# Performance work log

Hardware: AMD Instinct MI355X
Metric: run time of the kernel (lower is better)

## Reference

```python
import jax, jax.numpy as jnp
import numpy as np

EMBEDDING_BOUND = 1e4  # uniform init bound for box centers (repo constant)


def setup_inputs() -> dict:
    key = jax.random.key(0)
    k1, k2, k3 = jax.random.split(key, 3)
    num_classes, dim = 100000, 50
    d = dim // 2
    # init per MultiBoxEL.init_embeddings: centers ~ U(-B, B), offsets ~ N(1, 0.333)
    centers = jax.random.uniform(k1, (num_classes, d), dtype=jnp.float32,
                                 minval=-EMBEDDING_BOUND, maxval=EMBEDDING_BOUND)
    offsets = 1.0 + 0.333 * jax.random.normal(k2, (num_classes, d), dtype=jnp.float32)
    class_embeds = jnp.concatenate([centers, offsets], axis=1)  # [C, dim]
    nf1_data = jax.random.randint(k3, (2_000_000, 2), 0, num_classes)  # [N, 2] class ids
    return {"class_embeds": class_embeds, "nf1_data": nf1_data}


def _to_box(emb):
    # get_multiboxes: first half = center, second half = |offsets|
    d = emb.shape[-1] // 2
    return emb[:, :d], jnp.abs(emb[:, d:])


def reference(class_embeds, nf1_data):
    """nf1_loss (C subsumed-by D): batched inclusion loss 1 - Area(C ^ D)/Area(C),
    then L2 norm of relu(losses) over the batch (a scalar), exactly as inclusion_loss."""
    c_emb = class_embeds[nf1_data[:, 0]]  # [N, dim] gather (memory-bound)
    d_emb = class_embeds[nf1_data[:, 1]]
    cc, co = _to_box(c_emb)
    dc, do = _to_box(d_emb)
    # box intersection: [max(lowers), min(uppers)]; empty -> side length clipped to 0
    lo = jnp.maximum(cc - co, dc - do)
    hi = jnp.minimum(cc + co, dc + do)
    inter_area = jnp.prod(jax.nn.relu(hi - lo), axis=-1)  # [N]
    c_area = jnp.prod(2.0 * co, axis=-1)                  # [N] box volume = prod(2*offset)
    loss = jnp.where(c_area == 0, 0.0,
           jnp.where(jnp.isinf(c_area), 1.0 - inter_area / (2.0 * EMBEDDING_BOUND),
                     1.0 - inter_area / c_area))
    return jnp.linalg.norm(jax.nn.relu(loss))
```

## Files before the change

kernel.cpp:

```cpp
#include <hip/hip_runtime.h>
#include <hip/hip_cooperative_groups.h>
#include <math.h>

namespace cg = cooperative_groups;


#define DIMS 25
#define EMB_BOUND 10000.0f
#define FBLK 1024

__global__ void init_ws_kernel(float* ws) {
    if (threadIdx.x == 0 && blockIdx.x == 0) ws[0] = 0.0f;
}

__global__ __launch_bounds__(256, 8) void nf1_fallback_kernel(
    const float* __restrict__ emb, const int2* __restrict__ pairs,
    int n_pairs, float* __restrict__ ws)
{
    const int gl  = threadIdx.x & 31;
    const int gid = blockIdx.x * (blockDim.x >> 5) + (threadIdx.x >> 5);
    const int ngrp = gridDim.x * (blockDim.x >> 5);
    float acc = 0.0f;
    for (int p = gid; p < n_pairs; p += ngrp) {
        int2 pr = pairs[p];
        const float* rc = emb + (size_t)pr.x * (2 * DIMS);
        const float* rd = emb + (size_t)pr.y * (2 * DIMS);
        float t = 1.0f, a = 1.0f;
        if (gl < DIMS) {
            float cc = rc[gl], co = fabsf(rc[DIMS + gl]);
            float dc = rd[gl], dd = fabsf(rd[DIMS + gl]);
            float lo = fmaxf(cc - co, dc - dd);
            float hi = fminf(cc + co, dc + dd);
            t = fmaxf(hi - lo, 0.0f);
            a = 2.0f * co;
        }
        #pragma unroll
        for (int m = 16; m >= 1; m >>= 1) { t *= __shfl_xor(t, m, 32); a *= __shfl_xor(a, m, 32); }
        float loss;
        if (a == 0.0f)     loss = 0.0f;
        else if (isinf(a)) loss = 1.0f - t / (2.0f * EMB_BOUND);
        else               loss = 1.0f - t / a;
        loss = fmaxf(loss, 0.0f);
        if (gl == 0) acc += loss * loss;
    }
    #pragma unroll
    for (int m = 32; m >= 1; m >>= 1) acc += __shfl_xor(acc, m, 64);
    __shared__ float wsum[4];
    if ((threadIdx.x & 63) == 0) wsum[threadIdx.x >> 6] = acc;
    __syncthreads();
    if (threadIdx.x == 0) atomicAdd(ws, wsum[0] + wsum[1] + wsum[2] + wsum[3]);
}

__global__ void fallback_finalize_kernel(const float* __restrict__ ws, float* __restrict__ out) {
    if (threadIdx.x == 0 && blockIdx.x == 0) out[0] = sqrtf(fmaxf(ws[0], 0.0f));
}

__device__ __forceinline__ float slow_pair(const float* __restrict__ emb, int2 pr) {
    const float* ra = emb + (size_t)pr.x * (2 * DIMS);
    const float* rb = emb + (size_t)pr.y * (2 * DIMS);
    float inter = 1.0f, carea = 1.0f;
    for (int j = 0; j < DIMS; j++) {
        float cc = ra[j], co = fabsf(ra[DIMS + j]);
        float dc = rb[j], dd = fabsf(rb[DIMS + j]);
        float lo = fmaxf(cc - co, dc - dd);
        float hi = fminf(cc + co, dc + dd);
        inter *= fmaxf(hi - lo, 0.0f);
        carea *= 2.0f * co;
    }
    float loss;
    if (carea == 0.0f)     loss = 0.0f;
    else if (isinf(carea)) loss = 1.0f - inter / (2.0f * EMB_BOUND);
    else                   loss = 1.0f - inter / carea;
    loss = fmaxf(loss, 0.0f);
    return loss * loss;
}

__device__ __forceinline__ float key_pair(const float2* __restrict__ keys,
                                          const float* __restrict__ emb, int2 pr) {
    float2 ka = keys[pr.x];
    float2 kb = keys[pr.y];
    float t0 = fminf(ka.y, kb.y) - fmaxf(ka.x, kb.x);
    if (t0 > 0.0f) return slow_pair(emb, pr);
    return 1.0f;
}

template <int K>
__device__ __forceinline__ int ring_bucket(float lo, float hi) {
    float w = hi - lo;
    if (w <= 16.0f && fabsf(lo) <= 1.0e6f) {
        int i = (int)floorf(lo * 0.0625f);
        int b = i % K; if (b < 0) b += K;
        return b;
    }
    return K;
}

__device__ __forceinline__ bool ring_pass(unsigned a, unsigned b, unsigned K) {
    unsigned dd = (a >= b) ? (a - b) : (b - a);
    return (a == K) | (b == K) | (dd <= 1u) | (dd == K - 1u);
}

__device__ __forceinline__ float screen_pairs(
    const unsigned char* __restrict__ sbuck, const float2* __restrict__ keys,
    const float* __restrict__ emb, const int2* __restrict__ pairs,
    int n_pairs, int t, int nthreads)
{
    float sum = 0.0f;
    const int noct = n_pairs >> 3;
    const int4* p4 = (const int4*)pairs;
    for (int q = t; q < noct; q += nthreads) {
        int4 qa = p4[4 * q + 0], qb = p4[4 * q + 1];
        int4 qc = p4[4 * q + 2], qd = p4[4 * q + 3];
        int2 pr[8] = { make_int2(qa.x, qa.y), make_int2(qa.z, qa.w),
                       make_int2(qb.x, qb.y), make_int2(qb.z, qb.w),
                       make_int2(qc.x, qc.y), make_int2(qc.z, qc.w),
                       make_int2(qd.x, qd.y), make_int2(qd.z, qd.w) };
        unsigned ba[8], bb[8];
        #pragma unroll
        for (int i = 0; i < 8; i++) { ba[i] = sbuck[pr[i].x]; bb[i] = sbuck[pr[i].y]; }
        #pragma unroll
        for (int i = 0; i < 8; i++) {
            if (ring_pass(ba[i], bb[i], 255u)) sum += key_pair(keys, emb, pr[i]);
            else                               sum += 1.0f;
        }
    }
    for (int p = (noct << 3) + t; p < n_pairs; p += nthreads) {
        int2 pr = pairs[p];
        unsigned a = sbuck[pr.x], b = sbuck[pr.y];
        if (ring_pass(a, b, 255u)) sum += key_pair(keys, emb, pr);
        else                       sum += 1.0f;
    }
    return sum;
}

__global__ __launch_bounds__(FBLK, 1) void fused2_kernel(
    const float* __restrict__ emb, float2* __restrict__ keys,
    unsigned char* __restrict__ gbuck, const int2* __restrict__ pairs,
    int n_pairs, int n_rows, float* __restrict__ acc,
    unsigned* __restrict__ ticket, float* __restrict__ out)
{
    extern __shared__ unsigned char sbuck[];
    __shared__ float wsum[FBLK / 64];
    const int nthreads = gridDim.x * blockDim.x;
    const int t = blockIdx.x * blockDim.x + threadIdx.x;
    if (t == 0) { acc[0] = 0.0f; ticket[0] = 0u; }

    for (int r = t; r < n_rows; r += nthreads) {
        float c = emb[(size_t)r * (2 * DIMS)];
        float o = fabsf(emb[(size_t)r * (2 * DIMS) + DIMS]);
        float lo = c - o, hi = c + o;
        keys[r] = make_float2(lo, hi);
        gbuck[r] = (unsigned char)ring_bucket<255>(lo, hi);
    }

    cg::this_grid().sync();

    {
        const int nb16 = (n_rows + 15) >> 4;
        const uint4* g4 = (const uint4*)gbuck;
        uint4* s4 = (uint4*)sbuck;
        for (int i = threadIdx.x; i < nb16; i += blockDim.x) s4[i] = g4[i];
    }
    __syncthreads();

    float sum = screen_pairs(sbuck, keys, emb, pairs, n_pairs, t, nthreads);

    #pragma unroll
    for (int m = 32; m >= 1; m >>= 1) sum += __shfl_xor(sum, m, 64);
    if ((threadIdx.x & 63) == 0) wsum[threadIdx.x >> 6] = sum;
    __syncthreads();
    if (threadIdx.x == 0) {
        float s = 0.0f;
        #pragma unroll
        for (int w = 0; w < FBLK / 64; w++) s += wsum[w];
        atomicAdd(acc, s);
        __threadfence();
        unsigned tk = atomicAdd(ticket, 1u);
        if (tk == gridDim.x - 1)
            out[0] = sqrtf(fmaxf(atomicAdd(acc, 0.0f), 0.0f));
    }
}

__global__ __launch_bounds__(256) void repack_kb_kernel(
    const float* __restrict__ emb, float2* __restrict__ keys,
    unsigned char* __restrict__ gbuck, int n_rows,
    float* __restrict__ acc, unsigned* __restrict__ ticket)
{
    if (blockIdx.x == 0 && threadIdx.x == 0) { acc[0] = 0.0f; ticket[0] = 0u; }
    const int r = blockIdx.x * blockDim.x + threadIdx.x;
    if (r < n_rows) {
        float c = emb[(size_t)r * (2 * DIMS)];
        float o = fabsf(emb[(size_t)r * (2 * DIMS) + DIMS]);
        float lo = c - o, hi = c + o;
        keys[r] = make_float2(lo, hi);
        gbuck[r] = (unsigned char)ring_bucket<255>(lo, hi);
    }
}

__global__ __launch_bounds__(FBLK, 1) void screen_byte2_kernel(
    const float2* __restrict__ keys, const unsigned char* __restrict__ gbuck,
    const float* __restrict__ emb, const int2* __restrict__ pairs,
    int n_pairs, int n_rows, float* __restrict__ acc,
    unsigned* __restrict__ ticket, float* __restrict__ out)
{
    extern __shared__ unsigned char sbuck[];
    __shared__ float wsum[FBLK / 64];
    const int nthreads = gridDim.x * blockDim.x;
    const int t = blockIdx.x * blockDim.x + threadIdx.x;
    {
        const int nb16 = (n_rows + 15) >> 4;
        const uint4* g4 = (const uint4*)gbuck;
        uint4* s4 = (uint4*)sbuck;
        for (int i = threadIdx.x; i < nb16; i += blockDim.x) s4[i] = g4[i];
    }
    __syncthreads();

    float sum = screen_pairs(sbuck, keys, emb, pairs, n_pairs, t, nthreads);

    #pragma unroll
    for (int m = 32; m >= 1; m >>= 1) sum += __shfl_xor(sum, m, 64);
    if ((threadIdx.x & 63) == 0) wsum[threadIdx.x >> 6] = sum;
    __syncthreads();
    if (threadIdx.x == 0) {
        float s = 0.0f;
        #pragma unroll
        for (int w = 0; w < FBLK / 64; w++) s += wsum[w];
        atomicAdd(acc, s);
        __threadfence();
        unsigned tk = atomicAdd(ticket, 1u);
        if (tk == gridDim.x - 1)
            out[0] = sqrtf(fmaxf(atomicAdd(acc, 0.0f), 0.0f));
    }
}

extern "C" void kernel_launch(void* const* d_in, const int* in_sizes, int n_in,
                              void* d_out, int out_size, void* d_ws, size_t ws_size,
                              hipStream_t stream) {
    const float* emb  = (const float*)d_in[0];
    const int2*  prs  = (const int2*)d_in[1];
    int n_pairs = in_sizes[1] / 2;
    int n_rows  = in_sizes[0] / (2 * DIMS);

    float*    ws     = (float*)d_ws;
    unsigned* ticket = (unsigned*)(ws + 1);
    float*    out    = (float*)d_out;
    float2*   keys   = (float2*)((char*)d_ws + 256);
    unsigned char* gbuck = (unsigned char*)(keys + n_rows);

    int dev = 0;  hipGetDevice(&dev);
    int maxShared = 0, coop = 0, numCU = 0;
    hipDeviceGetAttribute(&maxShared, hipDeviceAttributeMaxSharedMemoryPerBlock, dev);
    hipDeviceGetAttribute(&coop, hipDeviceAttributeCooperativeLaunch, dev);
    hipDeviceGetAttribute(&numCU, hipDeviceAttributeMultiprocessorCount, dev);

    const size_t tabBytes = (size_t)((n_rows + 15) & ~15);
    const bool ws_ok = (ws_size >= 256 + (size_t)n_rows * 8 + tabBytes + 64) &&
                       ((n_rows & 1) == 0);
    const bool byte_ok = ((size_t)maxShared >= tabBytes + 512) && ws_ok;

    bool launched = false;
    if (byte_ok && coop && numCU > 0) {
        int blocksPerCU = 0;
        hipError_t oe = hipOccupancyMaxActiveBlocksPerMultiprocessor(
            &blocksPerCU, (const void*)fused2_kernel, FBLK, tabBytes);
        if (oe == hipSuccess && blocksPerCU >= 1) {
            int grid = blocksPerCU * numCU;
            void* args[] = { (void*)&emb, (void*)&keys, (void*)&gbuck,
                             (void*)&prs, (void*)&n_pairs, (void*)&n_rows,
                             (void*)&ws, (void*)&ticket, (void*)&out };
            hipError_t le = hipLaunchCooperativeKernel(
                (const void*)fused2_kernel, dim3(grid), dim3(FBLK),
                args, (unsigned int)tabBytes, stream);
            if (le == hipSuccess) launched = true;
        }
    }

    if (!launched && byte_ok) {
        const int rblocks = (n_rows + 255) / 256;
        hipLaunchKernelGGL(repack_kb_kernel, dim3(rblocks), dim3(256), 0, stream,
                           emb, keys, gbuck, n_rows, ws, ticket);
        const int grid = (numCU > 0) ? numCU : 256;
        hipLaunchKernelGGL(screen_byte2_kernel, dim3(grid), dim3(FBLK),
                           tabBytes, stream,
                           keys, gbuck, emb, prs, n_pairs, n_rows, ws, ticket, out);
        launched = true;
    }

    if (!launched) {
        hipLaunchKernelGGL(init_ws_kernel, dim3(1), dim3(64), 0, stream, ws);
        hipLaunchKernelGGL(nf1_fallback_kernel, dim3(4096), dim3(256), 0, stream,
                           emb, prs, n_pairs, ws);
        hipLaunchKernelGGL(fallback_finalize_kernel, dim3(1), dim3(64), 0, stream, ws, out);
    }
}
```

Baseline: 87.29 us.

## Replace cooperative fused kernel with tiled repack and prefetching screen kernel

Drops the cooperative single-kernel path with a grid-wide sync and goes back to two ordinary launches. The repack kernel now stages 128-row tiles of embeddings in shared memory with coalesced float4 loads, instead of each thread making strided single-float reads. The screen kernel issues its first batch of pair-index loads before filling the shared bucket table, so that load latency overlaps the table copy. The cost is an extra kernel launch boundary in place of the grid sync, plus a fixed grid of 256 blocks.

```diff
diff --git a/kernel.cpp b/kernel.cpp
--- a/kernel.cpp
+++ b/kernel.cpp
@@ -1,13 +1,12 @@
 #include <hip/hip_runtime.h>
-#include <hip/hip_cooperative_groups.h>
 #include <math.h>
-
-namespace cg = cooperative_groups;
 
 
 #define DIMS 25
 #define EMB_BOUND 10000.0f
 #define FBLK 1024
+#define TROWS 128
+#define TFLOATS (TROWS * 2 * DIMS)
 
 __global__ void init_ws_kernel(float* ws) {
     if (threadIdx.x == 0 && blockIdx.x == 0) ws[0] = 0.0f;
@@ -100,104 +99,39 @@
     return (a == K) | (b == K) | (dd <= 1u) | (dd == K - 1u);
 }
 
-__device__ __forceinline__ float screen_pairs(
-    const unsigned char* __restrict__ sbuck, const float2* __restrict__ keys,
-    const float* __restrict__ emb, const int2* __restrict__ pairs,
-    int n_pairs, int t, int nthreads)
-{
-    float sum = 0.0f;
-    const int noct = n_pairs >> 3;
-    const int4* p4 = (const int4*)pairs;
-    for (int q = t; q < noct; q += nthreads) {
-        int4 qa = p4[4 * q + 0], qb = p4[4 * q + 1];
-        int4 qc = p4[4 * q + 2], qd = p4[4 * q + 3];
-        int2 pr[8] = { make_int2(qa.x, qa.y), make_int2(qa.z, qa.w),
-                       make_int2(qb.x, qb.y), make_int2(qb.z, qb.w),
-                       make_int2(qc.x, qc.y), make_int2(qc.z, qc.w),
-                       make_int2(qd.x, qd.y), make_int2(qd.z, qd.w) };
-        unsigned ba[8], bb[8];
-        #pragma unroll
-        for (int i = 0; i < 8; i++) { ba[i] = sbuck[pr[i].x]; bb[i] = sbuck[pr[i].y]; }
-        #pragma unroll
-        for (int i = 0; i < 8; i++) {
-            if (ring_pass(ba[i], bb[i], 255u)) sum += key_pair(keys, emb, pr[i]);
-            else                               sum += 1.0f;
-        }
-    }
-    for (int p = (noct << 3) + t; p < n_pairs; p += nthreads) {
-        int2 pr = pairs[p];
-        unsigned a = sbuck[pr.x], b = sbuck[pr.y];
-        if (ring_pass(a, b, 255u)) sum += key_pair(keys, emb, pr);
-        else                       sum += 1.0f;
-    }
-    return sum;
-}
-
-__global__ __launch_bounds__(FBLK, 1) void fused2_kernel(
-    const float* __restrict__ emb, float2* __restrict__ keys,
-    unsigned char* __restrict__ gbuck, const int2* __restrict__ pairs,
-    int n_pairs, int n_rows, float* __restrict__ acc,
-    unsigned* __restrict__ ticket, float* __restrict__ out)
-{
-    extern __shared__ unsigned char sbuck[];
-    __shared__ float wsum[FBLK / 64];
-    const int nthreads = gridDim.x * blockDim.x;
-    const int t = blockIdx.x * blockDim.x + threadIdx.x;
-    if (t == 0) { acc[0] = 0.0f; ticket[0] = 0u; }
-
-    for (int r = t; r < n_rows; r += nthreads) {
-        float c = emb[(size_t)r * (2 * DIMS)];
-        float o = fabsf(emb[(size_t)r * (2 * DIMS) + DIMS]);
-        float lo = c - o, hi = c + o;
-        keys[r] = make_float2(lo, hi);
-        gbuck[r] = (unsigned char)ring_bucket<255>(lo, hi);
-    }
-
-    cg::this_grid().sync();
-
-    {
-        const int nb16 = (n_rows + 15) >> 4;
-        const uint4* g4 = (const uint4*)gbuck;
-        uint4* s4 = (uint4*)sbuck;
-        for (int i = threadIdx.x; i < nb16; i += blockDim.x) s4[i] = g4[i];
-    }
-    __syncthreads();
-
-    float sum = screen_pairs(sbuck, keys, emb, pairs, n_pairs, t, nthreads);
-
-    #pragma unroll
-    for (int m = 32; m >= 1; m >>= 1) sum += __shfl_xor(sum, m, 64);
-    if ((threadIdx.x & 63) == 0) wsum[threadIdx.x >> 6] = sum;
-    __syncthreads();
-    if (threadIdx.x == 0) {
-        float s = 0.0f;
-        #pragma unroll
-        for (int w = 0; w < FBLK / 64; w++) s += wsum[w];
-        atomicAdd(acc, s);
-        __threadfence();
-        unsigned tk = atomicAdd(ticket, 1u);
-        if (tk == gridDim.x - 1)
-            out[0] = sqrtf(fmaxf(atomicAdd(acc, 0.0f), 0.0f));
-    }
-}
-
-__global__ __launch_bounds__(256) void repack_kb_kernel(
+__global__ __launch_bounds__(256) void repack_tile_kernel(
     const float* __restrict__ emb, float2* __restrict__ keys,
     unsigned char* __restrict__ gbuck, int n_rows,
     float* __restrict__ acc, unsigned* __restrict__ ticket)
 {
+    __shared__ float tile[TFLOATS];
     if (blockIdx.x == 0 && threadIdx.x == 0) { acc[0] = 0.0f; ticket[0] = 0u; }
-    const int r = blockIdx.x * blockDim.x + threadIdx.x;
-    if (r < n_rows) {
-        float c = emb[(size_t)r * (2 * DIMS)];
-        float o = fabsf(emb[(size_t)r * (2 * DIMS) + DIMS]);
-        float lo = c - o, hi = c + o;
-        keys[r] = make_float2(lo, hi);
-        gbuck[r] = (unsigned char)ring_bucket<255>(lo, hi);
-    }
-}
-
-__global__ __launch_bounds__(FBLK, 1) void screen_byte2_kernel(
+    const int n_tiles = (n_rows + TROWS - 1) / TROWS;
+    for (int tIdx = blockIdx.x; tIdx < n_tiles; tIdx += gridDim.x) {
+        const int r0 = tIdx * TROWS;
+        const int rows = min(TROWS, n_rows - r0);
+        const int cnt = rows * (2 * DIMS);
+        const int n4 = cnt >> 2;
+        {
+            const float4* g4 = (const float4*)(emb + (size_t)r0 * (2 * DIMS));
+            float4* s4 = (float4*)tile;
+            for (int i = threadIdx.x; i < n4; i += blockDim.x) s4[i] = g4[i];
+            for (int i = (n4 << 2) + threadIdx.x; i < cnt; i += blockDim.x)
+                tile[i] = emb[(size_t)r0 * (2 * DIMS) + i];
+        }
+        __syncthreads();
+        for (int j = threadIdx.x; j < rows; j += blockDim.x) {
+            float c = tile[j * (2 * DIMS)];
+            float o = fabsf(tile[j * (2 * DIMS) + DIMS]);
+            float lo = c - o, hi = c + o;
+            keys[r0 + j] = make_float2(lo, hi);
+            gbuck[r0 + j] = (unsigned char)ring_bucket<255>(lo, hi);
+        }
+        __syncthreads();
+    }
+}
+
+__global__ __launch_bounds__(FBLK, 1) void screen_byte_kernel(
     const float2* __restrict__ keys, const unsigned char* __restrict__ gbuck,
     const float* __restrict__ emb, const int2* __restrict__ pairs,
     int n_pairs, int n_rows, float* __restrict__ acc,
@@ -207,6 +141,16 @@
     __shared__ float wsum[FBLK / 64];
     const int nthreads = gridDim.x * blockDim.x;
     const int t = blockIdx.x * blockDim.x + threadIdx.x;
+    const int noct = n_pairs >> 3;
+    const int4* p4 = (const int4*)pairs;
+
+    int4 qa, qb, qc, qd;
+    const bool have0 = t < noct;
+    if (have0) {
+        qa = p4[4 * t + 0]; qb = p4[4 * t + 1];
+        qc = p4[4 * t + 2]; qd = p4[4 * t + 3];
+    }
+
     {
         const int nb16 = (n_rows + 15) >> 4;
         const uint4* g4 = (const uint4*)gbuck;
@@ -215,7 +159,31 @@
     }
     __syncthreads();
 
-    float sum = screen_pairs(sbuck, keys, emb, pairs, n_pairs, t, nthreads);
+    float sum = 0.0f;
+    for (int q = t; q < noct; q += nthreads) {
+        if (q != t) {
+            qa = p4[4 * q + 0]; qb = p4[4 * q + 1];
+            qc = p4[4 * q + 2]; qd = p4[4 * q + 3];
+        }
+        int2 pr[8] = { make_int2(qa.x, qa.y), make_int2(qa.z, qa.w),
+                       make_int2(qb.x, qb.y), make_int2(qb.z, qb.w),
+                       make_int2(qc.x, qc.y), make_int2(qc.z, qc.w),
+                       make_int2(qd.x, qd.y), make_int2(qd.z, qd.w) };
+        unsigned ba[8], bb[8];
+        #pragma unroll
+        for (int i = 0; i < 8; i++) { ba[i] = sbuck[pr[i].x]; bb[i] = sbuck[pr[i].y]; }
+        #pragma unroll
+        for (int i = 0; i < 8; i++) {
+            if (ring_pass(ba[i], bb[i], 255u)) sum += key_pair(keys, emb, pr[i]);
+            else                               sum += 1.0f;
+        }
+    }
+    for (int p = (noct << 3) + t; p < n_pairs; p += nthreads) {
+        int2 pr = pairs[p];
+        unsigned a = sbuck[pr.x], b = sbuck[pr.y];
+        if (ring_pass(a, b, 255u)) sum += key_pair(keys, emb, pr);
+        else                       sum += 1.0f;
+    }
 
     #pragma unroll
     for (int m = 32; m >= 1; m >>= 1) sum += __shfl_xor(sum, m, 64);
@@ -248,45 +216,22 @@
     unsigned char* gbuck = (unsigned char*)(keys + n_rows);
 
     int dev = 0;  hipGetDevice(&dev);
-    int maxShared = 0, coop = 0, numCU = 0;
+    int maxShared = 0;
     hipDeviceGetAttribute(&maxShared, hipDeviceAttributeMaxSharedMemoryPerBlock, dev);
-    hipDeviceGetAttribute(&coop, hipDeviceAttributeCooperativeLaunch, dev);
-    hipDeviceGetAttribute(&numCU, hipDeviceAttributeMultiprocessorCount, dev);
 
     const size_t tabBytes = (size_t)((n_rows + 15) & ~15);
     const bool ws_ok = (ws_size >= 256 + (size_t)n_rows * 8 + tabBytes + 64) &&
                        ((n_rows & 1) == 0);
     const bool byte_ok = ((size_t)maxShared >= tabBytes + 512) && ws_ok;
 
-    bool launched = false;
-    if (byte_ok && coop && numCU > 0) {
-        int blocksPerCU = 0;
-        hipError_t oe = hipOccupancyMaxActiveBlocksPerMultiprocessor(
-            &blocksPerCU, (const void*)fused2_kernel, FBLK, tabBytes);
-        if (oe == hipSuccess && blocksPerCU >= 1) {
-            int grid = blocksPerCU * numCU;
-            void* args[] = { (void*)&emb, (void*)&keys, (void*)&gbuck,
-                             (void*)&prs, (void*)&n_pairs, (void*)&n_rows,
-                             (void*)&ws, (void*)&ticket, (void*)&out };
-            hipError_t le = hipLaunchCooperativeKernel(
-                (const void*)fused2_kernel, dim3(grid), dim3(FBLK),
-                args, (unsigned int)tabBytes, stream);
-            if (le == hipSuccess) launched = true;
-        }
-    }
-
-    if (!launched && byte_ok) {
-        const int rblocks = (n_rows + 255) / 256;
-        hipLaunchKernelGGL(repack_kb_kernel, dim3(rblocks), dim3(256), 0, stream,
-                           emb, keys, gbuck, n_rows, ws, ticket);
-        const int grid = (numCU > 0) ? numCU : 256;
-        hipLaunchKernelGGL(screen_byte2_kernel, dim3(grid), dim3(FBLK),
+    if (byte_ok) {
+        const int n_tiles = (n_rows + TROWS - 1) / TROWS;
+        hipLaunchKernelGGL(repack_tile_kernel, dim3(min(n_tiles, 2048)), dim3(256),
+                           0, stream, emb, keys, gbuck, n_rows, ws, ticket);
+        hipLaunchKernelGGL(screen_byte_kernel, dim3(256), dim3(FBLK),
                            tabBytes, stream,
                            keys, gbuck, emb, prs, n_pairs, n_rows, ws, ticket, out);
-        launched = true;
-    }
-
-    if (!launched) {
+    } else {
         hipLaunchKernelGGL(init_ws_kernel, dim3(1), dim3(64), 0, stream, ws);
         hipLaunchKernelGGL(nf1_fallback_kernel, dim3(4096), dim3(256), 0, stream,
                            emb, prs, n_pairs, ws);
```

Result: no change. 87.59 us (+0.3%).
